# Kernel tuning notes

Measured on AMD Instinct MI355X. Metric: run time of the kernel, lower is better.

Reference implementation:

```python
import jax, jax.numpy as jnp
import numpy as np

SPECIES = (0, 1)
CUTOFF = 6.0
N_ATOMS, N_EDGES, N_TRIPLETS = 20000, 500000, 2000000

G2_ETAS = np.array([0.003214, 0.035711, 0.071421, 0.124987, 0.214264, 0.357106, 0.714213, 1.428426], dtype=np.float32)
G4_ETAS = np.array([0.000357, 0.028569, 0.089277], dtype=np.float32)
G4_ZETAS = np.array([1.0, 2.0, 4.0], dtype=np.float32)
G4_LMDAS = np.array([-1.0, 1.0], dtype=np.float32)


def setup_inputs() -> dict:
    key = jax.random.key(0)
    ks = jax.random.split(key, 6)
    atomic_numbers = jax.random.randint(ks[0], (N_ATOMS,), 0, 2, dtype=jnp.int32)
    edge_index = jax.random.randint(ks[1], (2, N_EDGES), 0, N_ATOMS, dtype=jnp.int32)
    D_st = jax.random.uniform(ks[2], (N_EDGES,), minval=0.5, maxval=6.5, dtype=jnp.float32)
    id3_ba = jax.random.randint(ks[3], (N_TRIPLETS,), 0, N_EDGES, dtype=jnp.int32)
    id3_ca = jax.random.randint(ks[4], (N_TRIPLETS,), 0, N_EDGES, dtype=jnp.int32)
    cosphi = jax.random.uniform(ks[5], (N_TRIPLETS,), minval=-1.0, maxval=1.0, dtype=jnp.float32)
    # per-key parameters: 4 ordered species pairs for G2, 6 species triples for G4
    g2_etas = jnp.tile(jnp.asarray(G2_ETAS), (4, 1))
    g4_etas = jnp.tile(jnp.asarray(G4_ETAS), (6, 1))
    g4_zetas = jnp.tile(jnp.asarray(G4_ZETAS), (6, 1))
    g4_lmdas = jnp.tile(jnp.asarray(G4_LMDAS), (6, 1))
    return {"atomic_numbers": atomic_numbers, "edge_index": edge_index, "D_st": D_st,
            "id3_ba": id3_ba, "id3_ca": id3_ca, "cosphi": cosphi,
            "g2_etas": g2_etas, "g4_etas": g4_etas, "g4_zetas": g4_zetas, "g4_lmdas": g4_lmdas}


def _fc(R):
    # cosine cutoff (no in-range bool here; G4 applies its own range masks)
    return 0.5 * jnp.cos(jnp.pi * R / CUTOFF) + 0.5


def _acsf(atomic_numbers, edge_index, D_st, id3_ba, id3_ca, cosphi,
          g2_etas, g4_etas, g4_zetas, g4_lmdas):
    N = atomic_numbers.shape[0]
    dt = D_st.dtype
    src, tgt = edge_index[0], edge_index[1]
    an_src, an_tgt = atomic_numbers[src], atomic_numbers[tgt]

    # ---- triplet geometry (masking replaces boolean gather; scatter-add is equivalent) ----
    m3 = id3_ba > id3_ca                       # [T] triplet dedup mask
    R_ba = D_st[id3_ba]                        # [T]
    R_ca = D_st[id3_ca]
    sb = atomic_numbers[src[id3_ba]]           # species of edge-ba source
    tb = atomic_numbers[tgt[id3_ba]]           # species of central atom a
    sc = atomic_numbers[src[id3_ca]]
    seg3 = tgt[id3_ba]                         # scatter target: central atom index
    Rbc2 = R_ba * R_ba + R_ca * R_ca - 2.0 * R_ba * R_ca * cosphi
    R_bc = jnp.sqrt(jnp.maximum(Rbc2, 1e-12))
    in_range = ((R_bc < CUTOFF) & (R_ba < CUTOFF) & (R_ca < CUTOFF)).astype(dt)
    cut3 = _fc(R_ca) * _fc(R_bc) * _fc(R_ba) * in_range   # [T]
    r2sum = R_bc * R_bc + R_ba * R_ba + R_ca * R_ca       # [T]

    # ---- G2: per (source, target) species pair ----
    cut2 = _fc(D_st)                           # [E]
    d2 = D_st * D_st
    g2_per = {}
    k = 0
    for a1 in SPECIES:
        for a2 in SPECIES:
            w = ((an_tgt == a2) & (an_src == a1)).astype(dt)       # [E]
            res = (cut2 * w)[:, None] * jnp.exp(-g2_etas[k][None, :] * d2[:, None])  # [E,8]
            g2_per[(a1, a2)] = jax.ops.segment_sum(res, tgt, num_segments=N)        # [N,8]
            k += 1

    # ---- G4: per (a, b, c) species triple (b<=c) ----
    ns = len(SPECIES)
    g4_per = {}
    k = 0
    for a in SPECIES:
        for i in range(ns):
            b = SPECIES[i]
            for j in range(i, ns):
                c = SPECIES[j]
                idx = (((sb == b) & (tb == a) & (sc == c)) |
                       ((sb == c) & (tb == a) & (sc == b)))
                w = (m3 & idx).astype(dt)                                  # [T]
                eta, zta, lmda = g4_etas[k], g4_zetas[k], g4_lmdas[k]
                rad = jnp.exp(-eta[None, :] * r2sum[:, None])              # [T,3]
                cl = jnp.abs(1.0 + lmda[None, :, None] * cosphi[:, None, None]) ** zta[None, None, :]  # [T,2,3]
                res = cl[:, None, :, :] * rad[:, :, None, None] * (cut3 * w)[:, None, None, None]      # [T,3,2,3]
                g4 = jax.ops.segment_sum(res, seg3, num_segments=N)        # [N,3,2,3]
                g4_per[(a, b, c)] = (2.0 ** (1.0 - zta))[None, None, None, :] * g4
                k += 1

    # ---- assemble per-atom descriptor [N, 70]; rows carry their species' descriptor ----
    outs = []
    for a in SPECIES:
        mask = (atomic_numbers == a).astype(dt)[:, None]
        g2s = jnp.stack([g2_per[(s, a)] for s in SPECIES], axis=-1).reshape(N, -1)   # [N,16]
        trips = [(b, c) for i, b in enumerate(SPECIES) for c in SPECIES[i:]]
        g4s = jnp.stack([g4_per[(a, b, c)] for (b, c) in trips], axis=-1).reshape(N, -1)  # [N,54]
        outs.append(mask * jnp.concatenate([g2s, g4s], axis=-1))
    return outs[0] + outs[1]


def reference(atomic_numbers, edge_index, D_st, id3_ba, id3_ca, cosphi,
              g2_etas, g4_etas, g4_zetas, g4_lmdas):
    return _acsf(atomic_numbers, edge_index, D_st, id3_ba, id3_ca, cosphi,
                 g2_etas, g4_etas, g4_zetas, g4_lmdas)
```

## Files before the change

kernel.cpp:

```cpp
#include <hip/hip_runtime.h>


#define NSH    8
#define CAP_TS 16
#define CAP_ES 16

typedef int      vi2 __attribute__((ext_vector_type(2)));
typedef int      vi4 __attribute__((ext_vector_type(4)));
typedef float    vf2 __attribute__((ext_vector_type(2)));
typedef float    vf4 __attribute__((ext_vector_type(4)));
typedef unsigned vu2 __attribute__((ext_vector_type(2)));

static __device__ __forceinline__ float fc_dev(float R) {
    const float PI_OVER_CUT = 0.52359877559829887308f;
    return fmaf(0.5f, __cosf(PI_OVER_CUT * R), 0.5f);
}

static __device__ __forceinline__ unsigned enc_R(float d) {
    float u = rintf(d * (65535.0f / 8.0f));
    u = fminf(fmaxf(u, 0.0f), 65535.0f);
    return (unsigned)u;
}
static __device__ __forceinline__ float dec_R(unsigned pk) {
    return (float)(pk >> 16) * (8.0f / 65535.0f);
}


__global__ void edges_bin_kernel(const int* __restrict__ an,
                                 const int* __restrict__ ei,
                                 const float* __restrict__ D,
                                 const float* __restrict__ g2_etas,
                                 unsigned* __restrict__ epack,
                                 int* __restrict__ ecount,
                                 unsigned* __restrict__ erec,
                                 float* __restrict__ out, int E, int N) {
    int shard = blockIdx.x & (NSH - 1);
    int* __restrict__ ecnt = ecount + (size_t)shard * N;
    int i = blockIdx.x * blockDim.x + threadIdx.x;
    int e0 = i * 2;
    if (e0 >= E) return;

    int   srcs[2], tgts[2];
    float ds[2];
    int   nk;
    if (e0 + 1 < E) {
        vi2 sp = __builtin_nontemporal_load((const vi2*)ei + i);
        vi2 tp = __builtin_nontemporal_load((const vi2*)(ei + E) + i);
        vf2 dp = __builtin_nontemporal_load((const vf2*)D + i);
        srcs[0] = sp.x; srcs[1] = sp.y;
        tgts[0] = tp.x; tgts[1] = tp.y;
        ds[0] = dp.x;   ds[1] = dp.y;
        nk = 2;
    } else {
        srcs[0] = ei[e0]; tgts[0] = ei[E + e0]; ds[0] = D[e0];
        srcs[1] = 0;      tgts[1] = 0;          ds[1] = 0.0f;
        nk = 1;
    }
    int as[2];
#pragma unroll
    for (int k = 0; k < 2; ++k) as[k] = (k < nk) ? an[srcs[k]] : 0;
    unsigned pk[2];
#pragma unroll
    for (int k = 0; k < 2; ++k)
        pk[k] = (enc_R(ds[k]) << 16) | ((unsigned)tgts[k] << 1) | (unsigned)as[k];
    if (nk == 2) {
        vu2 pv; pv.x = pk[0]; pv.y = pk[1];
        *((vu2*)epack + i) = pv;
    } else {
        epack[e0] = pk[0];
    }
    float fcv[2];
#pragma unroll
    for (int k = 0; k < 2; ++k) fcv[k] = fc_dev(ds[k]);
    int slot[2];
#pragma unroll
    for (int k = 0; k < 2; ++k)
        slot[k] = (k < nk) ? atomicAdd(&ecnt[tgts[k]], 1) : CAP_ES;
#pragma unroll
    for (int k = 0; k < 2; ++k) {
        if (k >= nk) continue;
        if (slot[k] < CAP_ES) {
            unsigned fq = (unsigned)rintf(fminf(fmaxf(fcv[k], 0.0f), 1.0f) * 32767.0f);
            erec[((size_t)shard * N + tgts[k]) * CAP_ES + slot[k]] =
                (pk[k] & 0xFFFF0000u) | (fq << 1) | (pk[k] & 1u);
        } else {
            float d2 = ds[k] * ds[k];
            int at = an[tgts[k]];
            const float* eta = g2_etas + (as[k] * 2 + at) * 8;
            float* row = out + (size_t)tgts[k] * 70 + as[k];
#pragma unroll
            for (int q = 0; q < 8; ++q)
                atomicAdd(row + 2 * q, fcv[k] * __expf(-eta[q] * d2));
        }
    }
}

__global__ void trip_bin_kernel(const unsigned* __restrict__ epack,
                                const int* __restrict__ id3_ba,
                                const int* __restrict__ id3_ca,
                                const float* __restrict__ cosphi,
                                const int* __restrict__ an,
                                const float* __restrict__ g4_etas,
                                const float* __restrict__ g4_zetas,
                                const float* __restrict__ g4_lmdas,
                                int* __restrict__ tcount,
                                vf2* __restrict__ trec,
                                float* __restrict__ out, int T, int N) {
    int shard = blockIdx.x & (NSH - 1);
    int* __restrict__ tcnt = tcount + (size_t)shard * N;
    int i = blockIdx.x * blockDim.x + threadIdx.x;
    int t0 = i * 4;
    if (t0 >= T) return;

    int ba[4], ca[4];
    float cp[4];
    if (t0 + 3 < T) {
        vi4 b4 = __builtin_nontemporal_load((const vi4*)id3_ba + i);
        vi4 c4 = __builtin_nontemporal_load((const vi4*)id3_ca + i);
        vf4 p4 = __builtin_nontemporal_load((const vf4*)cosphi + i);
        ba[0] = b4.x; ba[1] = b4.y; ba[2] = b4.z; ba[3] = b4.w;
        ca[0] = c4.x; ca[1] = c4.y; ca[2] = c4.z; ca[3] = c4.w;
        cp[0] = p4.x; cp[1] = p4.y; cp[2] = p4.z; cp[3] = p4.w;
    } else {
#pragma unroll
        for (int k = 0; k < 4; ++k) {
            int t = t0 + k;
            ba[k] = (t < T) ? id3_ba[t] : 0;
            ca[k] = (t < T) ? id3_ca[t] : 1;
            cp[k] = (t < T) ? cosphi[t] : 0.0f;
        }
    }
    unsigned pb[4], pc[4];
    bool m[4];
#pragma unroll
    for (int k = 0; k < 4; ++k) {
        m[k] = ba[k] > ca[k];
        pb[k] = 0u; pc[k] = 0u;
        if (m[k]) {
            pb[k] = epack[ba[k]];
            pc[k] = epack[ca[k]];
        }
    }
    float Rba[4], Rca[4], Rm2[4];
    int seg[4];
    bool valid[4];
#pragma unroll
    for (int k = 0; k < 4; ++k) {
        Rba[k] = dec_R(pb[k]);
        Rca[k] = dec_R(pc[k]);
        float Rbc2 = Rba[k] * Rba[k] + Rca[k] * Rca[k]
                     - 2.0f * Rba[k] * Rca[k] * cp[k];
        Rm2[k] = fmaxf(Rbc2, 1e-12f);
        float Rbc = sqrtf(Rm2[k]);
        valid[k] = m[k] && (Rba[k] < 6.0f) && (Rca[k] < 6.0f) && (Rbc < 6.0f);
        seg[k] = (int)((pb[k] >> 1) & 0x7FFFu);
    }
    int slot[4];
#pragma unroll
    for (int k = 0; k < 4; ++k)
        slot[k] = valid[k] ? atomicAdd(&tcnt[seg[k]], 1) : CAP_TS;
#pragma unroll
    for (int k = 0; k < 4; ++k) {
        if (!valid[k]) continue;
        float r2sum = Rm2[k] + Rba[k] * Rba[k] + Rca[k] * Rca[k];
        float cut3 = fc_dev(Rba[k]) * fc_dev(Rca[k]) * fc_dev(sqrtf(Rm2[k]));
        int trip = (int)(pb[k] & 1u) + (int)(pc[k] & 1u);
        if (slot[k] < CAP_TS) {
            float cqf = fminf(fmaxf(fmaf(cp[k], 32767.5f, 32767.5f), 0.0f), 65535.0f);
            unsigned cq = (unsigned)rintf(cqf);
            unsigned c3q = (unsigned)rintf(cut3 * 16383.0f);
            unsigned w0 = (cq << 16) | (c3q << 2) | (unsigned)trip;
            vf2 r; r.x = __uint_as_float(w0); r.y = r2sum;
            trec[((size_t)shard * N + seg[k]) * CAP_TS + slot[k]] = r;
        } else {
            int A = an[seg[k]];
            int k4 = A * 3 + trip;
            const float* eta = g4_etas + k4 * 3;
            const float* zet = g4_zetas + k4 * 3;
            const float* lmd = g4_lmdas + k4 * 2;
            float rad[3];
#pragma unroll
            for (int e2 = 0; e2 < 3; ++e2)
                rad[e2] = __expf(-eta[e2] * r2sum) * cut3;
            float lg0 = __log2f(fabsf(fmaf(lmd[0], cp[k], 1.0f)));
            float lg1 = __log2f(fabsf(fmaf(lmd[1], cp[k], 1.0f)));
            float* row = out + (size_t)seg[k] * 70 + 16 + trip;
#pragma unroll
            for (int z = 0; z < 3; ++z) {
                float zv = zet[z], base = 1.0f - zv;
                float c0 = exp2f(fmaf(zv, lg0, base));
                float c1 = exp2f(fmaf(zv, lg1, base));
#pragma unroll
                for (int e2 = 0; e2 < 3; ++e2) {
                    atomicAdd(row + ((e2 * 2 + 0) * 3 + z) * 3, c0 * rad[e2]);
                    atomicAdd(row + ((e2 * 2 + 1) * 3 + z) * 3, c1 * rad[e2]);
                }
            }
        }
    }
}

__global__ __launch_bounds__(256) void gather_kernel(
        const int* __restrict__ an,
        const float* __restrict__ g2_etas,
        const float* __restrict__ g4_etas,
        const float* __restrict__ g4_zetas,
        const float* __restrict__ g4_lmdas,
        const int* __restrict__ tcount, const vf2* __restrict__ trec,
        const int* __restrict__ ecount, const unsigned* __restrict__ erec,
        float* __restrict__ out, int N) {
    __shared__ vf2      sg4[4][66];
    __shared__ unsigned sg2[4][64];
    int w = threadIdx.x >> 6;
    int lane = threadIdx.x & 63;
    int a = blockIdx.x * 4 + w;
    if (a >= N) return;
    int A = an[a];

    int c18 = lane % 18;
    int g3  = lane / 18;
    int g3r = (g3 > 2) ? 0 : g3;
    int z_c = c18 % 3;
    int l_c = (c18 / 3) % 2;
    int e_c = c18 / 6;
    float eta0, eta1, eta2w, zv0, zv1, zv2, lm0, lm1, lm2;
    {
        int k0 = A * 3 + 0, k1 = A * 3 + 1, k2 = A * 3 + 2;
        eta0 = g4_etas[k0 * 3 + e_c]; eta1 = g4_etas[k1 * 3 + e_c]; eta2w = g4_etas[k2 * 3 + e_c];
        zv0  = g4_zetas[k0 * 3 + z_c]; zv1 = g4_zetas[k1 * 3 + z_c]; zv2 = g4_zetas[k2 * 3 + z_c];
        lm0  = g4_lmdas[k0 * 2 + l_c]; lm1 = g4_lmdas[k1 * 2 + l_c]; lm2 = g4_lmdas[k2 * 2 + l_c];
    }
    auto zsel = [](float z) -> int {
        return (z == 1.0f) ? 0 : (z == 2.0f) ? 1 : (z == 4.0f) ? 2 : 3;
    };
    int zs0 = zsel(zv0), zs1 = zsel(zv1), zs2 = zsel(zv2);
    bool fastz = __all(zs0 < 3 && zs1 < 3 && zs2 < 3);

    int tcnt_[NSH];
#pragma unroll
    for (int q = 0; q < NSH; ++q)
        tcnt_[q] = min(tcount[(size_t)q * N + a], CAP_TS);
    int n_t = 0;
#pragma unroll
    for (int q = 0; q < NSH; ++q) n_t += tcnt_[q];

    float acc0 = 0.0f, acc1 = 0.0f, acc2 = 0.0f;
    vf2 zr; zr.x = 0.0f; zr.y = 0.0f;
    for (int b0 = 0; b0 < n_t; b0 += 64) {
        int nch = min(64, n_t - b0);
        vf2 rv = zr;
        if (lane < nch) {
            int loc = b0 + lane, s = 0;
            bool done = false;
#pragma unroll
            for (int q = 0; q < NSH - 1; ++q) {
                bool go = !done && (loc >= tcnt_[q]);
                loc  = go ? loc - tcnt_[q] : loc;
                s   += go ? 1 : 0;
                done = !go;
            }
            rv = trec[((size_t)s * N + a) * CAP_TS + loc];
        }
        sg4[w][lane] = rv;
        if (lane < 2) sg4[w][64 + lane] = zr;
        asm volatile("s_waitcnt lgkmcnt(0)" ::: "memory");
        int niter = (nch + 2) / 3;
        if (fastz) {
            for (int i = 0; i < niter; ++i) {
                vf2 b = sg4[w][i * 3 + g3r];
                unsigned w0 = __float_as_uint(b.x);
                int btr = (int)(w0 & 3u);
                float cut3 = (float)((w0 >> 2) & 0x3FFFu) * (1.0f / 16383.0f);
                float c = fmaf((float)(w0 >> 16), 2.0f / 65535.0f, -1.0f);
                float eta_r = (btr == 0) ? eta0 : (btr == 1) ? eta1 : eta2w;
                float lm_r  = (btr == 0) ? lm0  : (btr == 1) ? lm1  : lm2;
                int   zs_r  = (btr == 0) ? zs0  : (btr == 1) ? zs1  : zs2;
                float p1 = fabsf(fmaf(lm_r, c, 1.0f));
                float p2 = p1 * p1;
                float p4 = p2 * p2;
                float cl = (zs_r == 0) ? p1 : (zs_r == 1) ? p2 * 0.5f : p4 * 0.125f;
                float v = cl * __expf(-eta_r * b.y) * cut3;
                acc0 += (btr == 0) ? v : 0.0f;
                acc1 += (btr == 1) ? v : 0.0f;
                acc2 += (btr == 2) ? v : 0.0f;
            }
        } else {
            for (int i = 0; i < niter; ++i) {
                vf2 b = sg4[w][i * 3 + g3r];
                unsigned w0 = __float_as_uint(b.x);
                int btr = (int)(w0 & 3u);
                float cut3 = (float)((w0 >> 2) & 0x3FFFu) * (1.0f / 16383.0f);
                float c = fmaf((float)(w0 >> 16), 2.0f / 65535.0f, -1.0f);
                float eta_r = (btr == 0) ? eta0 : (btr == 1) ? eta1 : eta2w;
                float lm_r  = (btr == 0) ? lm0  : (btr == 1) ? lm1  : lm2;
                float zv_r  = (btr == 0) ? zv0  : (btr == 1) ? zv1  : zv2;
                float p1 = fabsf(fmaf(lm_r, c, 1.0f));
                float cl = exp2f(fmaf(zv_r, __log2f(p1), 1.0f - zv_r));
                float v = cl * __expf(-eta_r * b.y) * cut3;
                acc0 += (btr == 0) ? v : 0.0f;
                acc1 += (btr == 1) ? v : 0.0f;
                acc2 += (btr == 2) ? v : 0.0f;
            }
        }
    }
    {
        int cc = lane / 3;
        int tt = lane - cc * 3;
        float s0a = __shfl(acc0, cc),      s1a = __shfl(acc1, cc),      s2a = __shfl(acc2, cc);
        float s0b = __shfl(acc0, cc + 18), s1b = __shfl(acc1, cc + 18), s2b = __shfl(acc2, cc + 18);
        float s0c = __shfl(acc0, cc + 36), s1c = __shfl(acc1, cc + 36), s2c = __shfl(acc2, cc + 36);
        float va = (tt == 0) ? s0a : (tt == 1) ? s1a : s2a;
        float vb = (tt == 0) ? s0b : (tt == 1) ? s1b : s2b;
        float vc = (tt == 0) ? s0c : (tt == 1) ? s1c : s2c;
        if (lane < 54) out[(size_t)a * 70 + 16 + lane] += va + vb + vc;
    }

    int c16 = lane & 15;
    int g4g = lane >> 4;
    int s_c = c16 & 1;
    int i_c = c16 >> 1;
    float eta2 = g2_etas[(s_c * 2 + A) * 8 + i_c];
    int ecnt_[NSH];
#pragma unroll
    for (int q = 0; q < NSH; ++q)
        ecnt_[q] = min(ecount[(size_t)q * N + a], CAP_ES);
    int n_e = 0;
#pragma unroll
    for (int q = 0; q < NSH; ++q) n_e += ecnt_[q];

    float accg = 0.0f;
    for (int b0 = 0; b0 < n_e; b0 += 64) {
        int nch = min(64, n_e - b0);
        unsigned rv = 0u;
        if (lane < nch) {
            int loc = b0 + lane, s = 0;
            bool done = false;
#pragma unroll
            for (int q = 0; q < NSH - 1; ++q) {
                bool go = !done && (loc >= ecnt_[q]);
                loc  = go ? loc - ecnt_[q] : loc;
                s   += go ? 1 : 0;
                done = !go;
            }
            rv = erec[((size_t)s * N + a) * CAP_ES + loc];
        }
        sg2[w][lane] = rv;
        asm volatile("s_waitcnt lgkmcnt(0)" ::: "memory");
        int niter = (nch + 3) / 4;
        for (int i = 0; i < niter; ++i) {
            unsigned pk = sg2[w][i * 4 + g4g];
            int sp = (int)(pk & 1u);
            float d = dec_R(pk);
            float fcv = (float)((pk >> 1) & 0x7FFFu) * (1.0f / 32767.0f);
            float v = fcv * __expf(-eta2 * d * d);
            accg += (sp == s_c) ? v : 0.0f;
        }
    }
    {
        float r0 = __shfl(accg, lane);
        float r1 = __shfl(accg, lane + 16);
        float r2 = __shfl(accg, lane + 32);
        float r3 = __shfl(accg, lane + 48);
        if (lane < 16) out[(size_t)a * 70 + lane] += r0 + r1 + r2 + r3;
    }
}


__global__ void acsf_edges_kernel(const int* __restrict__ an,
                                  const int* __restrict__ ei,
                                  const float* __restrict__ D,
                                  const float* __restrict__ g2_etas,
                                  float2* __restrict__ edata,
                                  float* __restrict__ out,
                                  int E, int use_ws) {
    int e = blockIdx.x * blockDim.x + threadIdx.x;
    if (e >= E) return;
    float d = D[e];
    float cut2 = fc_dev(d);
    if (use_ws) edata[e] = make_float2(d, cut2);
    int src = ei[e];
    int tgt = ei[E + e];
    int as = an[src];
    int at = an[tgt];
    float d2 = d * d;
    const float* eta = g2_etas + (as * 2 + at) * 8;
    float* row = out + (size_t)tgt * 70 + as;
#pragma unroll
    for (int i = 0; i < 8; ++i)
        atomicAdd(row + 2 * i, cut2 * __expf(-eta[i] * d2));
}

__global__ void acsf_triplets_kernel(const int* __restrict__ an,
                                     const int* __restrict__ ei,
                                     const float* __restrict__ D,
                                     const float2* __restrict__ edata,
                                     const int* __restrict__ id3_ba,
                                     const int* __restrict__ id3_ca,
                                     const float* __restrict__ cosphi,
                                     const float* __restrict__ g4_etas,
                                     const float* __restrict__ g4_zetas,
                                     const float* __restrict__ g4_lmdas,
                                     float* __restrict__ out,
                                     int T, int E, int use_ws) {
    int t = blockIdx.x * blockDim.x + threadIdx.x;
    if (t >= T) return;
    int eba = id3_ba[t];
    int eca = id3_ca[t];
    if (eba <= eca) return;
    float R_ba, R_ca, fba, fca;
    if (use_ws) {
        float2 va = edata[eba];
        float2 vb = edata[eca];
        R_ba = va.x; fba = va.y;
        R_ca = vb.x; fca = vb.y;
    } else {
        R_ba = D[eba]; R_ca = D[eca];
        fba = fc_dev(R_ba); fca = fc_dev(R_ca);
    }
    if (R_ba >= 6.0f || R_ca >= 6.0f) return;
    float cph = cosphi[t];
    float Rbc2 = R_ba * R_ba + R_ca * R_ca - 2.0f * R_ba * R_ca * cph;
    float Rm2 = fmaxf(Rbc2, 1e-12f);
    float R_bc = sqrtf(Rm2);
    if (R_bc >= 6.0f) return;
    int seg = ei[E + eba];
    int A = an[seg];
    int sb = an[ei[eba]];
    int sc = an[ei[eca]];
    int trip = sb + sc;
    int k4 = A * 3 + trip;
    float cut3 = fba * fca * fc_dev(R_bc);
    float r2sum = Rm2 + R_ba * R_ba + R_ca * R_ca;
    const float* eta = g4_etas + k4 * 3;
    const float* zet = g4_zetas + k4 * 3;
    const float* lmd = g4_lmdas + k4 * 2;
    float rad[3];
#pragma unroll
    for (int e2 = 0; e2 < 3; ++e2)
        rad[e2] = __expf(-eta[e2] * r2sum) * cut3;
    float lg0 = __log2f(fabsf(fmaf(lmd[0], cph, 1.0f)));
    float lg1 = __log2f(fabsf(fmaf(lmd[1], cph, 1.0f)));
    float* row = out + (size_t)seg * 70 + 16 + trip;
#pragma unroll
    for (int z = 0; z < 3; ++z) {
        float zv = zet[z], bse = 1.0f - zv;
        float c0 = exp2f(fmaf(zv, lg0, bse));
        float c1 = exp2f(fmaf(zv, lg1, bse));
#pragma unroll
        for (int e2 = 0; e2 < 3; ++e2) {
            atomicAdd(row + ((e2 * 2 + 0) * 3 + z) * 3, c0 * rad[e2]);
            atomicAdd(row + ((e2 * 2 + 1) * 3 + z) * 3, c1 * rad[e2]);
        }
    }
}


extern "C" void kernel_launch(void* const* d_in, const int* in_sizes, int n_in,
                              void* d_out, int out_size, void* d_ws, size_t ws_size,
                              hipStream_t stream) {
    const int*   an       = (const int*)d_in[0];
    const int*   ei       = (const int*)d_in[1];
    const float* D        = (const float*)d_in[2];
    const int*   id3_ba   = (const int*)d_in[3];
    const int*   id3_ca   = (const int*)d_in[4];
    const float* cosphi   = (const float*)d_in[5];
    const float* g2_etas  = (const float*)d_in[6];
    const float* g4_etas  = (const float*)d_in[7];
    const float* g4_zetas = (const float*)d_in[8];
    const float* g4_lmdas = (const float*)d_in[9];
    (void)n_in;

    int N = in_sizes[0];
    int E = in_sizes[2];
    int T = in_sizes[3];
    float* out = (float*)d_out;

    size_t trec_b  = (size_t)NSH * N * CAP_TS * sizeof(vf2);
    size_t erec_b  = (size_t)NSH * N * CAP_ES * sizeof(unsigned);
    size_t epack_b = (size_t)((E + 3) & ~3) * sizeof(unsigned);
    size_t cnt_b   = (size_t)2 * NSH * N * sizeof(int);
    size_t need = trec_b + erec_b + epack_b + cnt_b;

    const int blk = 256;
    (void)hipMemsetAsync(d_out, 0, (size_t)out_size * sizeof(float), stream);

    if (ws_size >= need && N <= 32767) {
        char* p = (char*)d_ws;
        vf2*      trec  = (vf2*)p;             p += trec_b;
        unsigned* erec  = (unsigned*)p;        p += erec_b;
        unsigned* epack = (unsigned*)p;        p += epack_b;
        int*      tcount = (int*)p;
        int*      ecount = tcount + (size_t)NSH * N;
        (void)hipMemsetAsync(tcount, 0, cnt_b, stream);

        int ethreads = (E + 1) / 2;
        edges_bin_kernel<<<(ethreads + blk - 1) / blk, blk, 0, stream>>>(
            an, ei, D, g2_etas, epack, ecount, erec, out, E, N);
        int tthreads = (T + 3) / 4;
        trip_bin_kernel<<<(tthreads + blk - 1) / blk, blk, 0, stream>>>(
            epack, id3_ba, id3_ca, cosphi, an,
            g4_etas, g4_zetas, g4_lmdas, tcount, trec, out, T, N);
        gather_kernel<<<(N + 3) / 4, blk, 0, stream>>>(
            an, g2_etas, g4_etas, g4_zetas, g4_lmdas,
            tcount, trec, ecount, erec, out, N);
    } else {
        int use_ws = (ws_size >= (size_t)E * sizeof(float2)) ? 1 : 0;
        float2* edata = (float2*)d_ws;
        acsf_edges_kernel<<<(E + blk - 1) / blk, blk, 0, stream>>>(
            an, ei, D, g2_etas, edata, out, E, use_ws);
        acsf_triplets_kernel<<<(T + blk - 1) / blk, blk, 0, stream>>>(
            an, ei, D, edata, id3_ba, id3_ca, cosphi,
            g4_etas, g4_zetas, g4_lmdas, out, T, E, use_ws);
    }
}
```

Baseline: 188.5 us.

## Fuse binning and gather into one cooperative kernel and drop count sharding

Replaces the two memsets and three separate launches (edge binning, triplet binning, per-atom gather) with one cooperative persistent kernel. It zeroes the output and counters in-kernel and separates the phases with grid-wide syncs. It also removes the 8-way sharded per-atom counters in favour of a single counter per atom, with larger per-atom capacities. The aim is to cut launch and memset overhead and the shard-merge logic in the gather. In exchange, the unsharded counters concentrate atomic contention, and a fixed 1024-block grid may underuse or oversubscribe the device; a multi-kernel fallback runs if the cooperative launch fails.

```diff
diff --git a/kernel.cpp b/kernel.cpp
--- a/kernel.cpp
+++ b/kernel.cpp
@@ -1,9 +1,11 @@
 #include <hip/hip_runtime.h>
-
-
-#define NSH    8
-#define CAP_TS 16
-#define CAP_ES 16
+#include <hip/hip_cooperative_groups.h>
+
+namespace cg = cooperative_groups;
+
+
+#define CAP_T 96
+#define CAP_E 64
 
 typedef int      vi2 __attribute__((ext_vector_type(2)));
 typedef int      vi4 __attribute__((ext_vector_type(4)));
@@ -11,11 +13,30 @@
 typedef float    vf4 __attribute__((ext_vector_type(4)));
 typedef unsigned vu2 __attribute__((ext_vector_type(2)));
 
+struct Params {
+    const int*   an;
+    const int*   ei;
+    const float* D;
+    const int*   id3_ba;
+    const int*   id3_ca;
+    const float* cosphi;
+    const float* g2_etas;
+    const float* g4_etas;
+    const float* g4_zetas;
+    const float* g4_lmdas;
+    unsigned*    epack;
+    unsigned*    erec;
+    vf2*         trec;
+    int*         tcount;
+    int*         ecount;
+    float*       out;
+    int N, E, T;
+};
+
 static __device__ __forceinline__ float fc_dev(float R) {
     const float PI_OVER_CUT = 0.52359877559829887308f;
     return fmaf(0.5f, __cosf(PI_OVER_CUT * R), 0.5f);
 }
-
 static __device__ __forceinline__ unsigned enc_R(float d) {
     float u = rintf(d * (65535.0f / 8.0f));
     u = fminf(fmaxf(u, 0.0f), 65535.0f);
@@ -26,48 +47,36 @@
 }
 
 
-__global__ void edges_bin_kernel(const int* __restrict__ an,
-                                 const int* __restrict__ ei,
-                                 const float* __restrict__ D,
-                                 const float* __restrict__ g2_etas,
-                                 unsigned* __restrict__ epack,
-                                 int* __restrict__ ecount,
-                                 unsigned* __restrict__ erec,
-                                 float* __restrict__ out, int E, int N) {
-    int shard = blockIdx.x & (NSH - 1);
-    int* __restrict__ ecnt = ecount + (size_t)shard * N;
-    int i = blockIdx.x * blockDim.x + threadIdx.x;
+static __device__ __forceinline__ void edges_item(const Params& p, int i) {
     int e0 = i * 2;
-    if (e0 >= E) return;
-
     int   srcs[2], tgts[2];
     float ds[2];
     int   nk;
-    if (e0 + 1 < E) {
-        vi2 sp = __builtin_nontemporal_load((const vi2*)ei + i);
-        vi2 tp = __builtin_nontemporal_load((const vi2*)(ei + E) + i);
-        vf2 dp = __builtin_nontemporal_load((const vf2*)D + i);
+    if (e0 + 1 < p.E) {
+        vi2 sp = __builtin_nontemporal_load((const vi2*)p.ei + i);
+        vi2 tp = __builtin_nontemporal_load((const vi2*)(p.ei + p.E) + i);
+        vf2 dp = __builtin_nontemporal_load((const vf2*)p.D + i);
         srcs[0] = sp.x; srcs[1] = sp.y;
         tgts[0] = tp.x; tgts[1] = tp.y;
         ds[0] = dp.x;   ds[1] = dp.y;
         nk = 2;
     } else {
-        srcs[0] = ei[e0]; tgts[0] = ei[E + e0]; ds[0] = D[e0];
-        srcs[1] = 0;      tgts[1] = 0;          ds[1] = 0.0f;
+        srcs[0] = p.ei[e0]; tgts[0] = p.ei[p.E + e0]; ds[0] = p.D[e0];
+        srcs[1] = 0;        tgts[1] = 0;              ds[1] = 0.0f;
         nk = 1;
     }
     int as[2];
 #pragma unroll
-    for (int k = 0; k < 2; ++k) as[k] = (k < nk) ? an[srcs[k]] : 0;
+    for (int k = 0; k < 2; ++k) as[k] = (k < nk) ? p.an[srcs[k]] : 0;
     unsigned pk[2];
 #pragma unroll
     for (int k = 0; k < 2; ++k)
         pk[k] = (enc_R(ds[k]) << 16) | ((unsigned)tgts[k] << 1) | (unsigned)as[k];
     if (nk == 2) {
         vu2 pv; pv.x = pk[0]; pv.y = pk[1];
-        *((vu2*)epack + i) = pv;
+        *((vu2*)p.epack + i) = pv;
     } else {
-        epack[e0] = pk[0];
+        p.epack[e0] = pk[0];
     }
     float fcv[2];
 #pragma unroll
@@ -75,19 +84,19 @@
     int slot[2];
 #pragma unroll
     for (int k = 0; k < 2; ++k)
-        slot[k] = (k < nk) ? atomicAdd(&ecnt[tgts[k]], 1) : CAP_ES;
+        slot[k] = (k < nk) ? atomicAdd(&p.ecount[tgts[k]], 1) : CAP_E;
 #pragma unroll
     for (int k = 0; k < 2; ++k) {
         if (k >= nk) continue;
-        if (slot[k] < CAP_ES) {
+        if (slot[k] < CAP_E) {
             unsigned fq = (unsigned)rintf(fminf(fmaxf(fcv[k], 0.0f), 1.0f) * 32767.0f);
-            erec[((size_t)shard * N + tgts[k]) * CAP_ES + slot[k]] =
+            p.erec[(size_t)tgts[k] * CAP_E + slot[k]] =
                 (pk[k] & 0xFFFF0000u) | (fq << 1) | (pk[k] & 1u);
         } else {
             float d2 = ds[k] * ds[k];
-            int at = an[tgts[k]];
-            const float* eta = g2_etas + (as[k] * 2 + at) * 8;
-            float* row = out + (size_t)tgts[k] * 70 + as[k];
+            int at = p.an[tgts[k]];
+            const float* eta = p.g2_etas + (as[k] * 2 + at) * 8;
+            float* row = p.out + (size_t)tgts[k] * 70 + as[k];
 #pragma unroll
             for (int q = 0; q < 8; ++q)
                 atomicAdd(row + 2 * q, fcv[k] * __expf(-eta[q] * d2));
@@ -95,29 +104,14 @@
     }
 }
 
-__global__ void trip_bin_kernel(const unsigned* __restrict__ epack,
-                                const int* __restrict__ id3_ba,
-                                const int* __restrict__ id3_ca,
-                                const float* __restrict__ cosphi,
-                                const int* __restrict__ an,
-                                const float* __restrict__ g4_etas,
-                                const float* __restrict__ g4_zetas,
-                                const float* __restrict__ g4_lmdas,
-                                int* __restrict__ tcount,
-                                vf2* __restrict__ trec,
-                                float* __restrict__ out, int T, int N) {
-    int shard = blockIdx.x & (NSH - 1);
-    int* __restrict__ tcnt = tcount + (size_t)shard * N;
-    int i = blockIdx.x * blockDim.x + threadIdx.x;
+static __device__ __forceinline__ void trip_item(const Params& p, int i) {
     int t0 = i * 4;
-    if (t0 >= T) return;
-
     int ba[4], ca[4];
     float cp[4];
-    if (t0 + 3 < T) {
-        vi4 b4 = __builtin_nontemporal_load((const vi4*)id3_ba + i);
-        vi4 c4 = __builtin_nontemporal_load((const vi4*)id3_ca + i);
-        vf4 p4 = __builtin_nontemporal_load((const vf4*)cosphi + i);
+    if (t0 + 3 < p.T) {
+        vi4 b4 = __builtin_nontemporal_load((const vi4*)p.id3_ba + i);
+        vi4 c4 = __builtin_nontemporal_load((const vi4*)p.id3_ca + i);
+        vf4 p4 = __builtin_nontemporal_load((const vf4*)p.cosphi + i);
         ba[0] = b4.x; ba[1] = b4.y; ba[2] = b4.z; ba[3] = b4.w;
         ca[0] = c4.x; ca[1] = c4.y; ca[2] = c4.z; ca[3] = c4.w;
         cp[0] = p4.x; cp[1] = p4.y; cp[2] = p4.z; cp[3] = p4.w;
@@ -125,9 +119,9 @@
 #pragma unroll
         for (int k = 0; k < 4; ++k) {
             int t = t0 + k;
-            ba[k] = (t < T) ? id3_ba[t] : 0;
-            ca[k] = (t < T) ? id3_ca[t] : 1;
-            cp[k] = (t < T) ? cosphi[t] : 0.0f;
+            ba[k] = (t < p.T) ? p.id3_ba[t] : 0;
+            ca[k] = (t < p.T) ? p.id3_ca[t] : 1;
+            cp[k] = (t < p.T) ? p.cosphi[t] : 0.0f;
         }
     }
     unsigned pb[4], pc[4];
@@ -137,8 +131,8 @@
         m[k] = ba[k] > ca[k];
         pb[k] = 0u; pc[k] = 0u;
         if (m[k]) {
-            pb[k] = epack[ba[k]];
-            pc[k] = epack[ca[k]];
+            pb[k] = p.epack[ba[k]];
+            pc[k] = p.epack[ca[k]];
         }
     }
     float Rba[4], Rca[4], Rm2[4];
@@ -158,33 +152,33 @@
     int slot[4];
 #pragma unroll
     for (int k = 0; k < 4; ++k)
-        slot[k] = valid[k] ? atomicAdd(&tcnt[seg[k]], 1) : CAP_TS;
+        slot[k] = valid[k] ? atomicAdd(&p.tcount[seg[k]], 1) : CAP_T;
 #pragma unroll
     for (int k = 0; k < 4; ++k) {
         if (!valid[k]) continue;
         float r2sum = Rm2[k] + Rba[k] * Rba[k] + Rca[k] * Rca[k];
         float cut3 = fc_dev(Rba[k]) * fc_dev(Rca[k]) * fc_dev(sqrtf(Rm2[k]));
         int trip = (int)(pb[k] & 1u) + (int)(pc[k] & 1u);
-        if (slot[k] < CAP_TS) {
+        if (slot[k] < CAP_T) {
             float cqf = fminf(fmaxf(fmaf(cp[k], 32767.5f, 32767.5f), 0.0f), 65535.0f);
             unsigned cq = (unsigned)rintf(cqf);
             unsigned c3q = (unsigned)rintf(cut3 * 16383.0f);
             unsigned w0 = (cq << 16) | (c3q << 2) | (unsigned)trip;
             vf2 r; r.x = __uint_as_float(w0); r.y = r2sum;
-            trec[((size_t)shard * N + seg[k]) * CAP_TS + slot[k]] = r;
+            p.trec[(size_t)seg[k] * CAP_T + slot[k]] = r;
         } else {
-            int A = an[seg[k]];
+            int A = p.an[seg[k]];
             int k4 = A * 3 + trip;
-            const float* eta = g4_etas + k4 * 3;
-            const float* zet = g4_zetas + k4 * 3;
-            const float* lmd = g4_lmdas + k4 * 2;
+            const float* eta = p.g4_etas + k4 * 3;
+            const float* zet = p.g4_zetas + k4 * 3;
+            const float* lmd = p.g4_lmdas + k4 * 2;
             float rad[3];
 #pragma unroll
             for (int e2 = 0; e2 < 3; ++e2)
                 rad[e2] = __expf(-eta[e2] * r2sum) * cut3;
             float lg0 = __log2f(fabsf(fmaf(lmd[0], cp[k], 1.0f)));
             float lg1 = __log2f(fabsf(fmaf(lmd[1], cp[k], 1.0f)));
-            float* row = out + (size_t)seg[k] * 70 + 16 + trip;
+            float* row = p.out + (size_t)seg[k] * 70 + 16 + trip;
 #pragma unroll
             for (int z = 0; z < 3; ++z) {
                 float zv = zet[z], base = 1.0f - zv;
@@ -200,22 +194,10 @@
     }
 }
 
-__global__ __launch_bounds__(256) void gather_kernel(
-        const int* __restrict__ an,
-        const float* __restrict__ g2_etas,
-        const float* __restrict__ g4_etas,
-        const float* __restrict__ g4_zetas,
-        const float* __restrict__ g4_lmdas,
-        const int* __restrict__ tcount, const vf2* __restrict__ trec,
-        const int* __restrict__ ecount, const unsigned* __restrict__ erec,
-        float* __restrict__ out, int N) {
-    __shared__ vf2      sg4[4][66];
-    __shared__ unsigned sg2[4][64];
-    int w = threadIdx.x >> 6;
-    int lane = threadIdx.x & 63;
-    int a = blockIdx.x * 4 + w;
-    if (a >= N) return;
-    int A = an[a];
+static __device__ __forceinline__ void gather_atom(const Params& p, int a,
+                                                   int lane, vf2* s4,
+                                                   unsigned* s2) {
+    int A = p.an[a];
 
     int c18 = lane % 18;
     int g3  = lane / 18;
@@ -226,9 +208,9 @@
     float eta0, eta1, eta2w, zv0, zv1, zv2, lm0, lm1, lm2;
     {
         int k0 = A * 3 + 0, k1 = A * 3 + 1, k2 = A * 3 + 2;
-        eta0 = g4_etas[k0 * 3 + e_c]; eta1 = g4_etas[k1 * 3 + e_c]; eta2w = g4_etas[k2 * 3 + e_c];
-        zv0  = g4_zetas[k0 * 3 + z_c]; zv1 = g4_zetas[k1 * 3 + z_c]; zv2 = g4_zetas[k2 * 3 + z_c];
-        lm0  = g4_lmdas[k0 * 2 + l_c]; lm1 = g4_lmdas[k1 * 2 + l_c]; lm2 = g4_lmdas[k2 * 2 + l_c];
+        eta0 = p.g4_etas[k0 * 3 + e_c]; eta1 = p.g4_etas[k1 * 3 + e_c]; eta2w = p.g4_etas[k2 * 3 + e_c];
+        zv0  = p.g4_zetas[k0 * 3 + z_c]; zv1 = p.g4_zetas[k1 * 3 + z_c]; zv2 = p.g4_zetas[k2 * 3 + z_c];
+        lm0  = p.g4_lmdas[k0 * 2 + l_c]; lm1 = p.g4_lmdas[k1 * 2 + l_c]; lm2 = p.g4_lmdas[k2 * 2 + l_c];
     }
     auto zsel = [](float z) -> int {
         return (z == 1.0f) ? 0 : (z == 2.0f) ? 1 : (z == 4.0f) ? 2 : 3;
@@ -236,38 +218,21 @@
     int zs0 = zsel(zv0), zs1 = zsel(zv1), zs2 = zsel(zv2);
     bool fastz = __all(zs0 < 3 && zs1 < 3 && zs2 < 3);
 
-    int tcnt_[NSH];
-#pragma unroll
-    for (int q = 0; q < NSH; ++q)
-        tcnt_[q] = min(tcount[(size_t)q * N + a], CAP_TS);
-    int n_t = 0;
-#pragma unroll
-    for (int q = 0; q < NSH; ++q) n_t += tcnt_[q];
-
+    int n_t = min(p.tcount[a], CAP_T);
+    const vf2* rec = p.trec + (size_t)a * CAP_T;
     float acc0 = 0.0f, acc1 = 0.0f, acc2 = 0.0f;
     vf2 zr; zr.x = 0.0f; zr.y = 0.0f;
     for (int b0 = 0; b0 < n_t; b0 += 64) {
         int nch = min(64, n_t - b0);
         vf2 rv = zr;
-        if (lane < nch) {
-            int loc = b0 + lane, s = 0;
-            bool done = false;
-#pragma unroll
-            for (int q = 0; q < NSH - 1; ++q) {
-                bool go = !done && (loc >= tcnt_[q]);
-                loc  = go ? loc - tcnt_[q] : loc;
-                s   += go ? 1 : 0;
-                done = !go;
-            }
-            rv = trec[((size_t)s * N + a) * CAP_TS + loc];
-        }
-        sg4[w][lane] = rv;
-        if (lane < 2) sg4[w][64 + lane] = zr;
+        if (lane < nch) rv = __builtin_nontemporal_load(rec + b0 + lane);
+        s4[lane] = rv;
+        if (lane < 2) s4[64 + lane] = zr;
         asm volatile("s_waitcnt lgkmcnt(0)" ::: "memory");
         int niter = (nch + 2) / 3;
         if (fastz) {
             for (int i = 0; i < niter; ++i) {
-                vf2 b = sg4[w][i * 3 + g3r];
+                vf2 b = s4[i * 3 + g3r];
                 unsigned w0 = __float_as_uint(b.x);
                 int btr = (int)(w0 & 3u);
                 float cut3 = (float)((w0 >> 2) & 0x3FFFu) * (1.0f / 16383.0f);
@@ -286,7 +251,7 @@
             }
         } else {
             for (int i = 0; i < niter; ++i) {
-                vf2 b = sg4[w][i * 3 + g3r];
+                vf2 b = s4[i * 3 + g3r];
                 unsigned w0 = __float_as_uint(b.x);
                 int btr = (int)(w0 & 3u);
                 float cut3 = (float)((w0 >> 2) & 0x3FFFu) * (1.0f / 16383.0f);
@@ -312,43 +277,26 @@
         float va = (tt == 0) ? s0a : (tt == 1) ? s1a : s2a;
         float vb = (tt == 0) ? s0b : (tt == 1) ? s1b : s2b;
         float vc = (tt == 0) ? s0c : (tt == 1) ? s1c : s2c;
-        if (lane < 54) out[(size_t)a * 70 + 16 + lane] += va + vb + vc;
+        if (lane < 54) p.out[(size_t)a * 70 + 16 + lane] += va + vb + vc;
     }
 
     int c16 = lane & 15;
     int g4g = lane >> 4;
     int s_c = c16 & 1;
     int i_c = c16 >> 1;
-    float eta2 = g2_etas[(s_c * 2 + A) * 8 + i_c];
-    int ecnt_[NSH];
-#pragma unroll
-    for (int q = 0; q < NSH; ++q)
-        ecnt_[q] = min(ecount[(size_t)q * N + a], CAP_ES);
-    int n_e = 0;
-#pragma unroll
-    for (int q = 0; q < NSH; ++q) n_e += ecnt_[q];
-
+    float eta2 = p.g2_etas[(s_c * 2 + A) * 8 + i_c];
+    int n_e = min(p.ecount[a], CAP_E);
+    const unsigned* erc = p.erec + (size_t)a * CAP_E;
     float accg = 0.0f;
     for (int b0 = 0; b0 < n_e; b0 += 64) {
         int nch = min(64, n_e - b0);
         unsigned rv = 0u;
-        if (lane < nch) {
-            int loc = b0 + lane, s = 0;
-            bool done = false;
-#pragma unroll
-            for (int q = 0; q < NSH - 1; ++q) {
-                bool go = !done && (loc >= ecnt_[q]);
-                loc  = go ? loc - ecnt_[q] : loc;
-                s   += go ? 1 : 0;
-                done = !go;
-            }
-            rv = erec[((size_t)s * N + a) * CAP_ES + loc];
-        }
-        sg2[w][lane] = rv;
+        if (lane < nch) rv = __builtin_nontemporal_load(erc + b0 + lane);
+        s2[lane] = rv;
         asm volatile("s_waitcnt lgkmcnt(0)" ::: "memory");
         int niter = (nch + 3) / 4;
         for (int i = 0; i < niter; ++i) {
-            unsigned pk = sg2[w][i * 4 + g4g];
+            unsigned pk = s2[i * 4 + g4g];
             int sp = (int)(pk & 1u);
             float d = dec_R(pk);
             float fcv = (float)((pk >> 1) & 0x7FFFu) * (1.0f / 32767.0f);
@@ -361,10 +309,56 @@
         float r1 = __shfl(accg, lane + 16);
         float r2 = __shfl(accg, lane + 32);
         float r3 = __shfl(accg, lane + 48);
-        if (lane < 16) out[(size_t)a * 70 + lane] += r0 + r1 + r2 + r3;
-    }
-}
-
+        if (lane < 16) p.out[(size_t)a * 70 + lane] += r0 + r1 + r2 + r3;
+    }
+}
+
+__global__ __launch_bounds__(256, 4) void fused_kernel(Params p) {
+    cg::grid_group grid = cg::this_grid();
+    int tid  = blockIdx.x * blockDim.x + threadIdx.x;
+    int nthr = gridDim.x * blockDim.x;
+
+    int nz = p.N * 70;
+    for (int i = tid; i < nz; i += nthr) p.out[i] = 0.0f;
+    for (int i = tid; i < 2 * p.N; i += nthr) p.tcount[i] = 0;
+    grid.sync();
+
+    int eitems = (p.E + 1) / 2;
+    for (int i = tid; i < eitems; i += nthr) edges_item(p, i);
+    grid.sync();
+
+    int titems = (p.T + 3) / 4;
+    for (int i = tid; i < titems; i += nthr) trip_item(p, i);
+    grid.sync();
+
+    __shared__ vf2      sg4[4][66];
+    __shared__ unsigned sg2[4][64];
+    int w = threadIdx.x >> 6;
+    int lane = threadIdx.x & 63;
+    for (int a = blockIdx.x * 4 + w; a < p.N; a += gridDim.x * 4)
+        gather_atom(p, a, lane, sg4[w], sg2[w]);
+}
+
+__global__ __launch_bounds__(256) void edges_k(Params p) {
+    int tid = blockIdx.x * blockDim.x + threadIdx.x;
+    int stride = gridDim.x * blockDim.x;
+    int items = (p.E + 1) / 2;
+    for (int i = tid; i < items; i += stride) edges_item(p, i);
+}
+__global__ __launch_bounds__(256) void trip_k(Params p) {
+    int tid = blockIdx.x * blockDim.x + threadIdx.x;
+    int stride = gridDim.x * blockDim.x;
+    int items = (p.T + 3) / 4;
+    for (int i = tid; i < items; i += stride) trip_item(p, i);
+}
+__global__ __launch_bounds__(256) void gather_k(Params p) {
+    __shared__ vf2      sg4[4][66];
+    __shared__ unsigned sg2[4][64];
+    int w = threadIdx.x >> 6;
+    int lane = threadIdx.x & 63;
+    for (int a = blockIdx.x * 4 + w; a < p.N; a += gridDim.x * 4)
+        gather_atom(p, a, lane, sg4[w], sg2[w]);
+}
 
 __global__ void acsf_edges_kernel(const int* __restrict__ an,
                                   const int* __restrict__ ei,
@@ -475,35 +469,46 @@
     int T = in_sizes[3];
     float* out = (float*)d_out;
 
-    size_t trec_b  = (size_t)NSH * N * CAP_TS * sizeof(vf2);
-    size_t erec_b  = (size_t)NSH * N * CAP_ES * sizeof(unsigned);
+    size_t trec_b  = (size_t)N * CAP_T * sizeof(vf2);
     size_t epack_b = (size_t)((E + 3) & ~3) * sizeof(unsigned);
-    size_t cnt_b   = (size_t)2 * NSH * N * sizeof(int);
-    size_t need = trec_b + erec_b + epack_b + cnt_b;
+    size_t erec_b  = (size_t)N * CAP_E * sizeof(unsigned);
+    size_t cnt_b   = (size_t)2 * N * sizeof(int);
+    size_t need = trec_b + epack_b + erec_b + cnt_b;
 
     const int blk = 256;
-    (void)hipMemsetAsync(d_out, 0, (size_t)out_size * sizeof(float), stream);
 
     if (ws_size >= need && N <= 32767) {
-        char* p = (char*)d_ws;
-        vf2*      trec  = (vf2*)p;             p += trec_b;
-        unsigned* erec  = (unsigned*)p;        p += erec_b;
-        unsigned* epack = (unsigned*)p;        p += epack_b;
-        int*      tcount = (int*)p;
-        int*      ecount = tcount + (size_t)NSH * N;
-        (void)hipMemsetAsync(tcount, 0, cnt_b, stream);
-
-        int ethreads = (E + 1) / 2;
-        edges_bin_kernel<<<(ethreads + blk - 1) / blk, blk, 0, stream>>>(
-            an, ei, D, g2_etas, epack, ecount, erec, out, E, N);
-        int tthreads = (T + 3) / 4;
-        trip_bin_kernel<<<(tthreads + blk - 1) / blk, blk, 0, stream>>>(
-            epack, id3_ba, id3_ca, cosphi, an,
-            g4_etas, g4_zetas, g4_lmdas, tcount, trec, out, T, N);
-        gather_kernel<<<(N + 3) / 4, blk, 0, stream>>>(
-            an, g2_etas, g4_etas, g4_zetas, g4_lmdas,
-            tcount, trec, ecount, erec, out, N);
+        char* pws = (char*)d_ws;
+        vf2*      trec  = (vf2*)pws;           pws += trec_b;
+        unsigned* epack = (unsigned*)pws;      pws += epack_b;
+        unsigned* erec  = (unsigned*)pws;      pws += erec_b;
+        int*      tcount = (int*)pws;
+        int*      ecount = tcount + N;
+
+        Params prm;
+        prm.an = an; prm.ei = ei; prm.D = D;
+        prm.id3_ba = id3_ba; prm.id3_ca = id3_ca; prm.cosphi = cosphi;
+        prm.g2_etas = g2_etas; prm.g4_etas = g4_etas;
+        prm.g4_zetas = g4_zetas; prm.g4_lmdas = g4_lmdas;
+        prm.epack = epack; prm.erec = erec; prm.trec = trec;
+        prm.tcount = tcount; prm.ecount = ecount;
+        prm.out = out; prm.N = N; prm.E = E; prm.T = T;
+
+        void* args[] = { (void*)&prm };
+        hipError_t rc = hipLaunchCooperativeKernel(
+            (const void*)fused_kernel, dim3(1024), dim3(blk), args, 0, stream);
+        if (rc != hipSuccess) {
+            (void)hipMemsetAsync(d_out, 0, (size_t)out_size * sizeof(float), stream);
+            (void)hipMemsetAsync(tcount, 0, cnt_b, stream);
+            int egrid = ((E + 1) / 2 + blk - 1) / blk;
+            int tgrid = ((T + 3) / 4 + blk - 1) / blk;
+            int ggrid = (N + 3) / 4;
+            edges_k<<<egrid, blk, 0, stream>>>(prm);
+            trip_k<<<tgrid, blk, 0, stream>>>(prm);
+            gather_k<<<ggrid, blk, 0, stream>>>(prm);
+        }
     } else {
+        (void)hipMemsetAsync(d_out, 0, (size_t)out_size * sizeof(float), stream);
         int use_ws = (ws_size >= (size_t)E * sizeof(float2)) ? 1 : 0;
         float2* edata = (float2*)d_ws;
         acsf_edges_kernel<<<(E + blk - 1) / blk, blk, 0, stream>>>(
```

Result: slower. 596.4 us (+216.5%).
